# Kernel optimization log

Hardware: AMD Instinct MI355X
Metric: run time of the kernel (lower is better)

## Reference

```python
import jax, jax.numpy as jnp
import numpy as np
import math

B, N, DQ, DK, DV, H = 8, 1024, 512, 512, 512, 8


def setup_inputs() -> dict:
    key = jax.random.key(0)
    ks = jax.random.split(key, 9)
    s = 0.02
    return {
        "Q": jax.random.normal(ks[0], (B, N, DQ), jnp.float32),
        "K": jax.random.normal(ks[1], (B, N, DK), jnp.float32),
        "mask": jax.random.bernoulli(ks[2], 0.9, (B, N)).astype(jnp.float32),
        "Wq": jax.random.normal(ks[3], (DQ, DV), jnp.float32) * s,
        "bq": jnp.zeros((DV,), jnp.float32),
        "Wk": jax.random.normal(ks[4], (DK, DV), jnp.float32) * s,
        "bk": jnp.zeros((DV,), jnp.float32),
        "Wv": jax.random.normal(ks[5], (DK, DV), jnp.float32) * s,
        "bv": jnp.zeros((DV,), jnp.float32),
        "Wo": jax.random.normal(ks[6], (DV, DV), jnp.float32) * s,
        "bo": jnp.zeros((DV,), jnp.float32),
    }


def reference(Q, K, mask, Wq, bq, Wk, bk, Wv, bv, Wo, bo):
    b, n, _ = Q.shape
    dV = Wq.shape[1]
    dh = dV // H
    scale = 1.0 / math.sqrt(dV)
    m = mask[..., None]                      # [B,N,1]
    Qp = (Q @ Wq + bq) * m                   # [B,N,dV]
    Kp = (K @ Wk + bk) * m
    Vp = (K @ Wv + bv) * m
    # torch.cat(x.split(dh,2),0) == head-major stacking -> keep as [H,B,N,dh]
    q = Qp.reshape(b, n, H, dh).transpose(2, 0, 1, 3)
    k = Kp.reshape(b, n, H, dh).transpose(2, 0, 1, 3)
    v = Vp.reshape(b, n, H, dh).transpose(2, 0, 1, 3)
    S = jnp.einsum('hbnd,hbmd->hbnm', q, k) * scale   # [H,B,N,N]
    mx = jnp.max(S, axis=3, keepdims=True)            # unmasked row max (faithful)
    m1 = mask[None, :, :, None]                       # [1,B,N,1]
    m2 = mask[None, :, None, :]                       # [1,B,1,N]
    num = jnp.exp((S - mx) * m1 * m2) * m1 * m2
    A = num / (jnp.sum(num, axis=3, keepdims=True) + 1e-16)
    O = q + jnp.einsum('hbnm,hbmd->hbnd', A, v)       # residual on Q_
    O = O.transpose(1, 2, 0, 3).reshape(b, n, dV)     # un-split heads
    O = O + jax.nn.relu((O @ Wo + bo) * m)
    return O
```

## Files before the change

kernel.cpp:

```cpp
#include <hip/hip_runtime.h>

typedef short bf16x8 __attribute__((ext_vector_type(8)));
typedef float f32x4 __attribute__((ext_vector_type(4)));

#define MFMA16(a, b, c) __builtin_amdgcn_mfma_f32_16x16x32_bf16((a), (b), (c), 0, 0, 0)

#define GLOAD_LDS16(g, l)                                              \
  __builtin_amdgcn_global_load_lds(                                    \
      (const __attribute__((address_space(1))) unsigned int*)(g),      \
      (__attribute__((address_space(3))) unsigned int*)(l), 16, 0, 0)

__device__ __forceinline__ unsigned short f2b(float f) {
  union { float f; unsigned int u; } x; x.f = f;
  unsigned int r = x.u + 0x7FFFu + ((x.u >> 16) & 1u);
  return (unsigned short)(r >> 16);
}
__device__ __forceinline__ float b2f(unsigned short h) {
  union { unsigned int u; float f; } x; x.u = ((unsigned int)h) << 16;
  return x.f;
}
__device__ __forceinline__ unsigned int cvtpk(float lo, float hi) {
  unsigned int r;
  asm("v_cvt_pk_bf16_f32 %0, %1, %2" : "=v"(r) : "v"(lo), "v"(hi));
  return r;
}
__device__ __forceinline__ short cvt1(float x) {
  return (short)(unsigned short)cvtpk(x, x);
}
__device__ __forceinline__ float vexp2(float x) {
  float r;
  asm("v_exp_f32 %0, %1" : "=v"(r) : "v"(x));
  return r;
}

__global__ __launch_bounds__(256) void wtrans_kernel(
    const float* __restrict__ Wq, const float* __restrict__ Wk,
    const float* __restrict__ Wv, const float* __restrict__ Wo,
    short* __restrict__ Wt) {
  __shared__ float tile[64][65];
  const int z = blockIdx.z;
  const float* W = (z == 0) ? Wq : (z == 1) ? Wk : (z == 2) ? Wv : Wo;
  const int k0 = blockIdx.x * 64, n0 = blockIdx.y * 64;
  const int t = threadIdx.x;
  const int r = t >> 4, cc = (t & 15) * 4;
#pragma unroll
  for (int it = 0; it < 4; ++it) {
    int row = r + it * 16;
    const float4 v = *(const float4*)(W + (k0 + row) * 512 + n0 + cc);
    tile[row][cc + 0] = v.x; tile[row][cc + 1] = v.y;
    tile[row][cc + 2] = v.z; tile[row][cc + 3] = v.w;
  }
  __syncthreads();
  short* out = Wt + z * (512 * 512);
#pragma unroll
  for (int it = 0; it < 4; ++it) {
    int nrow = r + it * 16;
    unsigned int u0 = cvtpk(tile[cc + 0][nrow], tile[cc + 1][nrow]);
    unsigned int u1 = cvtpk(tile[cc + 2][nrow], tile[cc + 3][nrow]);
    uint2 uv; uv.x = u0; uv.y = u1;
    *(uint2*)(out + (n0 + nrow) * 512 + k0 + cc) = uv;
  }
}

__global__ __launch_bounds__(256) void cvt_kernel(
    const float* __restrict__ Q, const float* __restrict__ K,
    const float* __restrict__ mask,
    short* __restrict__ Qb, short* __restrict__ Kb, float* __restrict__ ml) {
  if (blockIdx.y == 0 && blockIdx.x < 4) {
    int i = (blockIdx.x * 256 + threadIdx.x) * 8;
    float4 a = *(const float4*)(mask + i);
    float4 bb = *(const float4*)(mask + i + 4);
    float4 ra, rb;
    ra.x = (a.x != 0.f) ? 0.f : -1e30f;
    ra.y = (a.y != 0.f) ? 0.f : -1e30f;
    ra.z = (a.z != 0.f) ? 0.f : -1e30f;
    ra.w = (a.w != 0.f) ? 0.f : -1e30f;
    rb.x = (bb.x != 0.f) ? 0.f : -1e30f;
    rb.y = (bb.y != 0.f) ? 0.f : -1e30f;
    rb.z = (bb.z != 0.f) ? 0.f : -1e30f;
    rb.w = (bb.w != 0.f) ? 0.f : -1e30f;
    *(float4*)(ml + i) = ra;
    *(float4*)(ml + i + 4) = rb;
  }
  const float* src = blockIdx.y ? K : Q;
  short* dst = blockIdx.y ? Kb : Qb;
  int i = (blockIdx.x * 256 + threadIdx.x) * 8;
  float4 v0 = *(const float4*)(src + i);
  float4 v1 = *(const float4*)(src + i + 4);
  uint2 a, b;
  a.x = cvtpk(v0.x, v0.y); a.y = cvtpk(v0.z, v0.w);
  b.x = cvtpk(v1.x, v1.y); b.y = cvtpk(v1.z, v1.w);
  *(uint2*)(dst + i) = a;
  *(uint2*)(dst + i + 4) = b;
}

__device__ __forceinline__ void gemm_bf16_core(
    const short* __restrict__ A, const short* __restrict__ Wt,
    short* Lb, int m0, int t, f32x4 acc[4][4]) {
  const int lane = t & 63, w = t >> 6;
  const int c = lane & 15, g = lane >> 4;
  const int wr = w >> 1, wc = w & 1;
  const int lr = lane >> 3;
  const int sswz = ((lane & 7) ^ lr) << 3;
  const int swc = (c & 7) << 3;
  short* Al = Lb;
  short* Bl = Lb + 8192;

  for (int kt = 0; kt < 8; ++kt) {
#pragma unroll
    for (int it = 0; it < 4; ++it) {
      int row = w * 32 + it * 8;
      GLOAD_LDS16(A + (size_t)(m0 + row + lr) * 512 + kt * 64 + sswz, Al + row * 64);
      GLOAD_LDS16(Wt + (size_t)(row + lr) * 512 + kt * 64 + sswz, Bl + row * 64);
    }
    __syncthreads();
    __builtin_amdgcn_s_setprio(1);
#pragma unroll
    for (int kc = 0; kc < 2; ++kc) {
      bf16x8 af[4], bfr[4];
#pragma unroll
      for (int mi = 0; mi < 4; ++mi) {
        int r = wr * 64 + mi * 16 + c;
        af[mi] = *(const bf16x8*)(Al + r * 64 + ((kc * 32 + 8 * g) ^ swc));
      }
#pragma unroll
      for (int ni = 0; ni < 4; ++ni) {
        int r = wc * 64 + ni * 16 + c;
        bfr[ni] = *(const bf16x8*)(Bl + r * 64 + ((kc * 32 + 8 * g) ^ swc));
      }
#pragma unroll
      for (int mi = 0; mi < 4; ++mi)
#pragma unroll
        for (int ni = 0; ni < 4; ++ni)
          acc[mi][ni] = MFMA16(af[mi], bfr[ni], acc[mi][ni]);
    }
    __builtin_amdgcn_s_setprio(0);
    __syncthreads();
  }
}

__global__ __launch_bounds__(256) void proj2_kernel(
    const short* __restrict__ Qb, const short* __restrict__ Kb,
    const short* __restrict__ Wt4,
    const float* __restrict__ bq, const float* __restrict__ bk, const float* __restrict__ bv,
    const float* __restrict__ maskf,
    short* __restrict__ Qp, short* __restrict__ Kp, short* __restrict__ Vt) {
  __shared__ short Lbuf[16384];
  const int by = blockIdx.y;
  const int m0 = blockIdx.x * 128;
  const int t = threadIdx.x;
  const short* A;
  const short* Wt;
  const float* bias;
  int nbase;
  if (by < 4) { A = Qb; nbase = by * 128; Wt = Wt4 + nbase * 512; bias = bq; }
  else if (by < 8) { A = Kb; nbase = (by - 4) * 128; Wt = Wt4 + 262144 + nbase * 512; bias = bk; }
  else { A = Kb; nbase = (by - 8) * 128; Wt = Wt4 + 524288 + nbase * 512; bias = bv; }

  const f32x4 zz = {0.f, 0.f, 0.f, 0.f};
  f32x4 acc[4][4];
#pragma unroll
  for (int mi = 0; mi < 4; ++mi)
#pragma unroll
    for (int ni = 0; ni < 4; ++ni) acc[mi][ni] = zz;
  gemm_bf16_core(A, Wt, Lbuf, m0, t, acc);

  const int lane = t & 63, w = t >> 6;
  const int c = lane & 15, g = lane >> 4;
  const int wr = w >> 1, wc = w & 1;
  float mk[4][4];
#pragma unroll
  for (int mi = 0; mi < 4; ++mi) {
    int mbase = m0 + wr * 64 + mi * 16 + 4 * g;
#pragma unroll
    for (int i = 0; i < 4; ++i) mk[mi][i] = maskf[mbase + i];
  }
  float bval[4];
#pragma unroll
  for (int ni = 0; ni < 4; ++ni) bval[ni] = bias[nbase + wc * 64 + ni * 16 + c];

  if (by < 8) {
#pragma unroll
    for (int ni = 0; ni < 4; ++ni) {
      int nloc = wc * 64 + ni * 16 + c;
#pragma unroll
      for (int mi = 0; mi < 4; ++mi) {
#pragma unroll
        for (int i = 0; i < 4; ++i) {
          int mloc = wr * 64 + mi * 16 + 4 * g + i;
          float v = (acc[mi][ni][i] + bval[ni]) * mk[mi][i];
          Lbuf[mloc * 128 + (nloc ^ ((mloc & 7) << 3))] = cvt1(v);
        }
      }
    }
    __syncthreads();
    short* outp = (by < 4) ? Qp : Kp;
    const int rrow = t >> 4, rcol = (t & 15) * 8;
#pragma unroll
    for (int p = 0; p < 8; ++p) {
      int m = p * 16 + rrow;
      bf16x8 vv = *(const bf16x8*)(Lbuf + m * 128 + (rcol ^ ((m & 7) << 3)));
      *(bf16x8*)(outp + (size_t)(m0 + m) * 512 + nbase + rcol) = vv;
    }
  } else {
#pragma unroll
    for (int ni = 0; ni < 4; ++ni) {
      int nloc = wc * 64 + ni * 16 + c;
#pragma unroll
      for (int mi = 0; mi < 4; ++mi) {
        int mloc4 = wr * 64 + mi * 16 + 4 * g;
        unsigned int lo = cvtpk((acc[mi][ni][0] + bval[ni]) * mk[mi][0],
                                (acc[mi][ni][1] + bval[ni]) * mk[mi][1]);
        unsigned int hi = cvtpk((acc[mi][ni][2] + bval[ni]) * mk[mi][2],
                                (acc[mi][ni][3] + bval[ni]) * mk[mi][3]);
        int ma = (mloc4 & 15) + (((mloc4 >> 4) ^ (nloc & 7)) << 4);
        uint2 uv; uv.x = lo; uv.y = hi;
        *(uint2*)(Lbuf + nloc * 128 + ma) = uv;
      }
    }
    __syncthreads();
    const int rrow = t >> 4, rcol = (t & 15) * 8;
#pragma unroll
    for (int p = 0; p < 8; ++p) {
      int n = p * 16 + rrow;
      int ma = (rcol & 8) + (((rcol >> 4) ^ (n & 7)) << 4);
      bf16x8 vv = *(const bf16x8*)(Lbuf + n * 128 + ma);
      int d = nbase + n;
      int hh = d >> 6, dd = d & 63;
      int mg = m0 + rcol;
      int bi = mg >> 10, seq0 = mg & 1023;
      *(bf16x8*)(Vt + ((size_t)((bi * 8 + hh) * 64 + dd)) * 1024 + seq0) = vv;
    }
  }
}

__global__ __launch_bounds__(128) void attn3_kernel(
    const short* __restrict__ Qp, const short* __restrict__ Kp,
    const short* __restrict__ Vt, const float* __restrict__ mask,
    const float* __restrict__ ml, short* __restrict__ Obb) {
  __shared__ short Kl[64][64];
  __shared__ short Vl[64][64];
  __shared__ short Pl[2][2][16][64];
  __shared__ float Mlds[1024];
  const int t = threadIdx.x, lane = t & 63, w = t >> 6;
  const int c = lane & 15, g = lane >> 4;
  const int hw = blockIdx.x;
  const int L = (hw & 7) * 128 + (hw >> 3);
  const int qt = L & 15, hb = L >> 4;
  const int b = hb & 7, h = hb >> 3;
  const int n0 = qt * 64;
  const float scale2 = 0.06375870724f;

  const short* Kg = Kp + (size_t)(b * 1024) * 512 + h * 64;
  const short* Vg = Vt + (size_t)((b * 8 + h) * 64) * 1024;
  const float* Lg = ml + b * 1024;
  const int sswz = ((lane & 7) ^ (lane >> 3)) << 3;
  const int swc = (c & 7) << 3;

  bf16x8 qf[2][2];
#pragma unroll
  for (int grp = 0; grp < 2; ++grp) {
    const short* qptr = Qp + ((size_t)(b * 1024 + n0 + w * 32 + grp * 16 + c) * 512 + h * 64 + 8 * g);
    qf[grp][0] = *(const bf16x8*)qptr;
    qf[grp][1] = *(const bf16x8*)(qptr + 32);
  }
  bf16x8 ones;
#pragma unroll
  for (int k = 0; k < 8; ++k) ones[k] = (short)0x3F80;

  auto STAGEKV = [&](int kvt) {
    const int kr = kvt * 64;
#pragma unroll
    for (int it = 0; it < 4; ++it) {
      int row = it * 16 + w * 8;
      GLOAD_LDS16(Kg + (size_t)(kr + row + (lane >> 3)) * 512 + sswz, &Kl[row][0]);
      GLOAD_LDS16(Vg + (size_t)(row + (lane >> 3)) * 1024 + kr + sswz, &Vl[row][0]);
    }
  };

  GLOAD_LDS16(Lg + w * 512 + lane * 4, &Mlds[w * 512]);
  GLOAD_LDS16(Lg + w * 512 + 256 + lane * 4, &Mlds[w * 512 + 256]);
  STAGEKV(0);
  __syncthreads();

  const f32x4 zz = {0.f, 0.f, 0.f, 0.f};
  f32x4 o[2][4];
  f32x4 suma[2];
#pragma unroll
  for (int grp = 0; grp < 2; ++grp) {
    suma[grp] = zz;
#pragma unroll
    for (int nb = 0; nb < 4; ++nb) o[grp][nb] = zz;
  }

#pragma unroll 1
  for (int kvt = 0; kvt < 16; ++kvt) {
    float4 lm[4];
#pragma unroll
    for (int j = 0; j < 4; ++j)
      lm[j] = *(const float4*)(&Mlds[kvt * 64 + 16 * j + 4 * g]);

    f32x4 sv[2][4];
    __builtin_amdgcn_s_setprio(1);
#pragma unroll
    for (int j = 0; j < 4; ++j) {
      bf16x8 af0 = *(const bf16x8*)(&Kl[16 * j + c][(8 * g) ^ swc]);
      bf16x8 af1 = *(const bf16x8*)(&Kl[16 * j + c][(32 + 8 * g) ^ swc]);
#pragma unroll
      for (int grp = 0; grp < 2; ++grp) {
        f32x4 sj = MFMA16(af0, qf[grp][0], zz);
        sv[grp][j] = MFMA16(af1, qf[grp][1], sj);
      }
    }
    __builtin_amdgcn_s_setprio(0);

#pragma unroll
    for (int grp = 0; grp < 2; ++grp) {
#pragma unroll
      for (int j = 0; j < 4; ++j) {
        float p0 = vexp2(fmaf(scale2, sv[grp][j][0], lm[j].x));
        float p1 = vexp2(fmaf(scale2, sv[grp][j][1], lm[j].y));
        float p2 = vexp2(fmaf(scale2, sv[grp][j][2], lm[j].z));
        float p3 = vexp2(fmaf(scale2, sv[grp][j][3], lm[j].w));
        uint2 pw; pw.x = cvtpk(p0, p1); pw.y = cvtpk(p2, p3);
        *(uint2*)(&Pl[w][grp][c][(16 * j + 4 * g) ^ swc]) = pw;
      }
    }

    __builtin_amdgcn_s_setprio(1);
#pragma unroll
    for (int ks = 0; ks < 2; ++ks) {
      bf16x8 vb[4];
#pragma unroll
      for (int nb = 0; nb < 4; ++nb)
        vb[nb] = *(const bf16x8*)(&Vl[16 * nb + c][(ks * 32 + 8 * g) ^ swc]);
#pragma unroll
      for (int grp = 0; grp < 2; ++grp) {
        bf16x8 pa = *(const bf16x8*)(&Pl[w][grp][c][(ks * 32 + 8 * g) ^ swc]);
        suma[grp] = MFMA16(pa, ones, suma[grp]);
#pragma unroll
        for (int nb = 0; nb < 4; ++nb)
          o[grp][nb] = MFMA16(pa, vb[nb], o[grp][nb]);
      }
    }
    __builtin_amdgcn_s_setprio(0);

    if (kvt < 15) {
      __syncthreads();
      STAGEKV(kvt + 1);
      __syncthreads();
    }
  }

#pragma unroll
  for (int grp = 0; grp < 2; ++grp) {
    float inv[4], mk1[4];
#pragma unroll
    for (int i = 0; i < 4; ++i) {
      inv[i] = __builtin_amdgcn_rcpf(suma[grp][i] + 1e-16f);
      mk1[i] = mask[b * 1024 + n0 + w * 32 + grp * 16 + 4 * g + i];
    }
#pragma unroll
    for (int nb = 0; nb < 4; ++nb) {
      int colg = h * 64 + 16 * nb + c;
#pragma unroll
      for (int i = 0; i < 4; ++i) {
        int row = n0 + w * 32 + grp * 16 + 4 * g + i;
        float att = o[grp][nb][i] * inv[i];
        float qv = b2f(*(const unsigned short*)(Qp + (size_t)(b * 1024 + row) * 512 + colg));
        float res = qv + mk1[i] * att;
        Obb[(size_t)(b * 1024 + row) * 512 + colg] = cvt1(res);
      }
    }
  }
}

__global__ __launch_bounds__(256) void final2_kernel(
    const short* __restrict__ Obb,
    const short* __restrict__ Wto, const float* __restrict__ bo,
    const float* __restrict__ maskf, float* __restrict__ out) {
  __shared__ short Lbuf[16384];
  const int m0 = blockIdx.x * 128, n0 = blockIdx.y * 128;
  const int t = threadIdx.x;
  const f32x4 zz = {0.f, 0.f, 0.f, 0.f};
  f32x4 acc[4][4];
#pragma unroll
  for (int mi = 0; mi < 4; ++mi)
#pragma unroll
    for (int ni = 0; ni < 4; ++ni) acc[mi][ni] = zz;
  gemm_bf16_core(Obb, Wto + n0 * 512, Lbuf, m0, t, acc);

  const int lane = t & 63, w = t >> 6;
  const int c = lane & 15, g = lane >> 4;
  const int wr = w >> 1, wc = w & 1;
  float mk[4][4];
#pragma unroll
  for (int mi = 0; mi < 4; ++mi) {
    int mbase = m0 + wr * 64 + mi * 16 + 4 * g;
#pragma unroll
    for (int i = 0; i < 4; ++i) mk[mi][i] = maskf[mbase + i];
  }
#pragma unroll
  for (int ni = 0; ni < 4; ++ni) {
    int n = n0 + wc * 64 + ni * 16 + c;
    float bval = bo[n];
#pragma unroll
    for (int mi = 0; mi < 4; ++mi) {
      int mbase = m0 + wr * 64 + mi * 16 + 4 * g;
#pragma unroll
      for (int i = 0; i < 4; ++i) {
        float v = (acc[mi][ni][i] + bval) * mk[mi][i];
        v = fmaxf(v, 0.f);
        size_t off = (size_t)(mbase + i) * 512 + n;
        out[off] = b2f((unsigned short)Obb[off]) + v;
      }
    }
  }
}

extern "C" void kernel_launch(void* const* d_in, const int* in_sizes, int n_in,
                              void* d_out, int out_size, void* d_ws, size_t ws_size,
                              hipStream_t stream) {
  (void)in_sizes; (void)n_in; (void)out_size; (void)ws_size;
  const float* Q    = (const float*)d_in[0];
  const float* K    = (const float*)d_in[1];
  const float* mask = (const float*)d_in[2];
  const float* Wq   = (const float*)d_in[3];
  const float* bq   = (const float*)d_in[4];
  const float* Wk   = (const float*)d_in[5];
  const float* bk   = (const float*)d_in[6];
  const float* Wv   = (const float*)d_in[7];
  const float* bv   = (const float*)d_in[8];
  const float* Wo   = (const float*)d_in[9];
  const float* bo   = (const float*)d_in[10];

  char* ws = (char*)d_ws;
  const size_t MB = 1048576;
  short* Wt4 = (short*)ws;
  short* Qb  = (short*)(ws + 2 * MB);
  short* Kb  = (short*)(ws + 10 * MB);
  short* Qp  = (short*)(ws + 18 * MB);
  short* Kp  = (short*)(ws + 26 * MB);
  short* Vt  = (short*)(ws + 34 * MB);
  short* Obb = (short*)(ws + 42 * MB);
  float* ml  = (float*)(ws + 50 * MB);
  float* out = (float*)d_out;

  wtrans_kernel<<<dim3(8, 8, 4), 256, 0, stream>>>(Wq, Wk, Wv, Wo, Wt4);
  cvt_kernel<<<dim3(2048, 2), 256, 0, stream>>>(Q, K, mask, Qb, Kb, ml);
  proj2_kernel<<<dim3(64, 12), 256, 0, stream>>>(Qb, Kb, Wt4, bq, bk, bv, mask, Qp, Kp, Vt);
  attn3_kernel<<<dim3(1024), 128, 0, stream>>>(Qp, Kp, Vt, mask, ml, Obb);
  final2_kernel<<<dim3(64, 4), 256, 0, stream>>>(Obb, Wt4 + 3 * 262144, bo, mask, out);
}
```

Baseline: 88.90 us.

## Rewrite attention with 32x32 MFMA single-wave tiles and register-resident probabilities

Replaces the two-wave 16x16 MFMA attention kernel with a one-wave-per-block kernel using 32x32x16 bf16 MFMA on 32-query tiles. The softmax scale is folded into the Wk weights and bias, so scores feed exp2 directly. The additive -1e30 mask is replaced by a bf16 0/1 mask vector used in an MFMA row-sum. This works because masked keys already project to zero K and V, so they add nothing to P·V. Probabilities are repacked across lanes with shuffles instead of going through LDS. The next K/V tile is prefetched right after the LDS reads, with no block barriers. The aim is to cut LDS traffic, syncs and MFMA issue count. The costs are halved blocks per tile, more waves to launch, and a transpose through LDS in the epilogue.

```diff
diff --git a/kernel.cpp b/kernel.cpp
--- a/kernel.cpp
+++ b/kernel.cpp
@@ -2,8 +2,10 @@
 
 typedef short bf16x8 __attribute__((ext_vector_type(8)));
 typedef float f32x4 __attribute__((ext_vector_type(4)));
+typedef float f32x16 __attribute__((ext_vector_type(16)));
 
 #define MFMA16(a, b, c) __builtin_amdgcn_mfma_f32_16x16x32_bf16((a), (b), (c), 0, 0, 0)
+#define MFMA32(a, b, c) __builtin_amdgcn_mfma_f32_32x32x16_bf16((a), (b), (c), 0, 0, 0)
 
 #define GLOAD_LDS16(g, l)                                              \
   __builtin_amdgcn_global_load_lds(                                    \
@@ -32,6 +34,8 @@
   asm("v_exp_f32 %0, %1" : "=v"(r) : "v"(x));
   return r;
 }
+
+#define SCALE2 0.06375870724f
 
 __global__ __launch_bounds__(256) void wtrans_kernel(
     const float* __restrict__ Wq, const float* __restrict__ Wk,
@@ -40,6 +44,7 @@
   __shared__ float tile[64][65];
   const int z = blockIdx.z;
   const float* W = (z == 0) ? Wq : (z == 1) ? Wk : (z == 2) ? Wv : Wo;
+  const float ws = (z == 1) ? SCALE2 : 1.0f;
   const int k0 = blockIdx.x * 64, n0 = blockIdx.y * 64;
   const int t = threadIdx.x;
   const int r = t >> 4, cc = (t & 15) * 4;
@@ -55,8 +60,8 @@
 #pragma unroll
   for (int it = 0; it < 4; ++it) {
     int nrow = r + it * 16;
-    unsigned int u0 = cvtpk(tile[cc + 0][nrow], tile[cc + 1][nrow]);
-    unsigned int u1 = cvtpk(tile[cc + 2][nrow], tile[cc + 3][nrow]);
+    unsigned int u0 = cvtpk(tile[cc + 0][nrow] * ws, tile[cc + 1][nrow] * ws);
+    unsigned int u1 = cvtpk(tile[cc + 2][nrow] * ws, tile[cc + 3][nrow] * ws);
     uint2 uv; uv.x = u0; uv.y = u1;
     *(uint2*)(out + (n0 + nrow) * 512 + k0 + cc) = uv;
   }
@@ -65,22 +70,23 @@
 __global__ __launch_bounds__(256) void cvt_kernel(
     const float* __restrict__ Q, const float* __restrict__ K,
     const float* __restrict__ mask,
-    short* __restrict__ Qb, short* __restrict__ Kb, float* __restrict__ ml) {
+    short* __restrict__ Qb, short* __restrict__ Kb, short* __restrict__ mbf) {
   if (blockIdx.y == 0 && blockIdx.x < 4) {
     int i = (blockIdx.x * 256 + threadIdx.x) * 8;
     float4 a = *(const float4*)(mask + i);
     float4 bb = *(const float4*)(mask + i + 4);
-    float4 ra, rb;
-    ra.x = (a.x != 0.f) ? 0.f : -1e30f;
-    ra.y = (a.y != 0.f) ? 0.f : -1e30f;
-    ra.z = (a.z != 0.f) ? 0.f : -1e30f;
-    ra.w = (a.w != 0.f) ? 0.f : -1e30f;
-    rb.x = (bb.x != 0.f) ? 0.f : -1e30f;
-    rb.y = (bb.y != 0.f) ? 0.f : -1e30f;
-    rb.z = (bb.z != 0.f) ? 0.f : -1e30f;
-    rb.w = (bb.w != 0.f) ? 0.f : -1e30f;
-    *(float4*)(ml + i) = ra;
-    *(float4*)(ml + i + 4) = rb;
+    unsigned int m0 = (a.x != 0.f) ? 0x3F80u : 0u;
+    unsigned int m1 = (a.y != 0.f) ? 0x3F80u : 0u;
+    unsigned int m2 = (a.z != 0.f) ? 0x3F80u : 0u;
+    unsigned int m3 = (a.w != 0.f) ? 0x3F80u : 0u;
+    unsigned int m4 = (bb.x != 0.f) ? 0x3F80u : 0u;
+    unsigned int m5 = (bb.y != 0.f) ? 0x3F80u : 0u;
+    unsigned int m6 = (bb.z != 0.f) ? 0x3F80u : 0u;
+    unsigned int m7 = (bb.w != 0.f) ? 0x3F80u : 0u;
+    uint4 mm;
+    mm.x = m0 | (m1 << 16); mm.y = m2 | (m3 << 16);
+    mm.z = m4 | (m5 << 16); mm.w = m6 | (m7 << 16);
+    *(uint4*)(mbf + i) = mm;
   }
   const float* src = blockIdx.y ? K : Q;
   short* dst = blockIdx.y ? Kb : Qb;
@@ -156,6 +162,7 @@
   if (by < 4) { A = Qb; nbase = by * 128; Wt = Wt4 + nbase * 512; bias = bq; }
   else if (by < 8) { A = Kb; nbase = (by - 4) * 128; Wt = Wt4 + 262144 + nbase * 512; bias = bk; }
   else { A = Kb; nbase = (by - 8) * 128; Wt = Wt4 + 524288 + nbase * 512; bias = bv; }
+  const float bscale = (by >= 4 && by < 8) ? SCALE2 : 1.0f;
 
   const f32x4 zz = {0.f, 0.f, 0.f, 0.f};
   f32x4 acc[4][4];
@@ -177,7 +184,7 @@
   }
   float bval[4];
 #pragma unroll
-  for (int ni = 0; ni < 4; ++ni) bval[ni] = bias[nbase + wc * 64 + ni * 16 + c];
+  for (int ni = 0; ni < 4; ++ni) bval[ni] = bias[nbase + wc * 64 + ni * 16 + c] * bscale;
 
   if (by < 8) {
 #pragma unroll
@@ -234,144 +241,165 @@
   }
 }
 
-__global__ __launch_bounds__(128) void attn3_kernel(
+__global__ __launch_bounds__(64) void attn4_kernel(
     const short* __restrict__ Qp, const short* __restrict__ Kp,
     const short* __restrict__ Vt, const float* __restrict__ mask,
-    const float* __restrict__ ml, short* __restrict__ Obb) {
+    const short* __restrict__ mbf, short* __restrict__ Obb) {
   __shared__ short Kl[64][64];
   __shared__ short Vl[64][64];
-  __shared__ short Pl[2][2][16][64];
-  __shared__ float Mlds[1024];
-  const int t = threadIdx.x, lane = t & 63, w = t >> 6;
-  const int c = lane & 15, g = lane >> 4;
+  __shared__ short Ml[1024];
+  __shared__ short Tl[32][68];
+  const int t = threadIdx.x;
+  const int q32 = t & 31, hi = t >> 5;
   const int hw = blockIdx.x;
-  const int L = (hw & 7) * 128 + (hw >> 3);
-  const int qt = L & 15, hb = L >> 4;
-  const int b = hb & 7, h = hb >> 3;
-  const int n0 = qt * 64;
-  const float scale2 = 0.06375870724f;
+  const int L = (hw & 7) * 256 + (hw >> 3);
+  const int qt = L & 31, head = L >> 5;
+  const int b = head & 7, h = head >> 3;
+  const int n0 = qt * 32;
 
   const short* Kg = Kp + (size_t)(b * 1024) * 512 + h * 64;
   const short* Vg = Vt + (size_t)((b * 8 + h) * 64) * 1024;
-  const float* Lg = ml + b * 1024;
-  const int sswz = ((lane & 7) ^ (lane >> 3)) << 3;
-  const int swc = (c & 7) << 3;
-
-  bf16x8 qf[2][2];
-#pragma unroll
-  for (int grp = 0; grp < 2; ++grp) {
-    const short* qptr = Qp + ((size_t)(b * 1024 + n0 + w * 32 + grp * 16 + c) * 512 + h * 64 + 8 * g);
-    qf[grp][0] = *(const bf16x8*)qptr;
-    qf[grp][1] = *(const bf16x8*)(qptr + 32);
-  }
-  bf16x8 ones;
-#pragma unroll
-  for (int k = 0; k < 8; ++k) ones[k] = (short)0x3F80;
-
-  auto STAGEKV = [&](int kvt) {
+  const int sswz = ((t & 7) ^ (t >> 3)) << 3;
+  const int rswz = (t & 7) << 3;
+
+  bf16x8 qf[4];
+  {
+    const short* qptr = Qp + ((size_t)(b * 1024 + n0 + q32) * 512 + h * 64 + 8 * hi);
+#pragma unroll
+    for (int kk = 0; kk < 4; ++kk) qf[kk] = *(const bf16x8*)(qptr + 16 * kk);
+  }
+
+  auto STAGE = [&](int kvt) {
     const int kr = kvt * 64;
 #pragma unroll
-    for (int it = 0; it < 4; ++it) {
-      int row = it * 16 + w * 8;
-      GLOAD_LDS16(Kg + (size_t)(kr + row + (lane >> 3)) * 512 + sswz, &Kl[row][0]);
-      GLOAD_LDS16(Vg + (size_t)(row + (lane >> 3)) * 1024 + kr + sswz, &Vl[row][0]);
+    for (int it = 0; it < 8; ++it) {
+      int row = it * 8;
+      GLOAD_LDS16(Kg + (size_t)(kr + row + (t >> 3)) * 512 + sswz, &Kl[row][0]);
+      GLOAD_LDS16(Vg + (size_t)(row + (t >> 3)) * 1024 + kr + sswz, &Vl[row][0]);
     }
   };
 
-  GLOAD_LDS16(Lg + w * 512 + lane * 4, &Mlds[w * 512]);
-  GLOAD_LDS16(Lg + w * 512 + 256 + lane * 4, &Mlds[w * 512 + 256]);
-  STAGEKV(0);
-  __syncthreads();
-
-  const f32x4 zz = {0.f, 0.f, 0.f, 0.f};
-  f32x4 o[2][4];
-  f32x4 suma[2];
-#pragma unroll
-  for (int grp = 0; grp < 2; ++grp) {
-    suma[grp] = zz;
-#pragma unroll
-    for (int nb = 0; nb < 4; ++nb) o[grp][nb] = zz;
-  }
+  GLOAD_LDS16(mbf + b * 1024 + t * 8, &Ml[0]);
+  GLOAD_LDS16(mbf + b * 1024 + 512 + t * 8, &Ml[512]);
+  STAGE(0);
+
+  f32x16 o0 = {0.f}, o1 = {0.f}, suma = {0.f};
+#pragma unroll
+  for (int e = 0; e < 16; ++e) { o0[e] = 0.f; o1[e] = 0.f; suma[e] = 0.f; }
 
 #pragma unroll 1
   for (int kvt = 0; kvt < 16; ++kvt) {
-    float4 lm[4];
-#pragma unroll
-    for (int j = 0; j < 4; ++j)
-      lm[j] = *(const float4*)(&Mlds[kvt * 64 + 16 * j + 4 * g]);
-
-    f32x4 sv[2][4];
+    asm volatile("s_waitcnt vmcnt(0)" ::: "memory");
+    __builtin_amdgcn_sched_barrier(0);
+
+    bf16x8 ka[2][4], va[2][4], mo[4];
+#pragma unroll
+    for (int nb = 0; nb < 2; ++nb)
+#pragma unroll
+      for (int kk = 0; kk < 4; ++kk)
+        ka[nb][kk] = *(const bf16x8*)(&Kl[32 * nb + q32][(16 * kk + 8 * hi) ^ rswz]);
+#pragma unroll
+    for (int ds = 0; ds < 2; ++ds)
+#pragma unroll
+      for (int kk = 0; kk < 4; ++kk)
+        va[ds][kk] = *(const bf16x8*)(&Vl[32 * ds + q32][(16 * kk + 8 * hi) ^ rswz]);
+#pragma unroll
+    for (int kk = 0; kk < 4; ++kk)
+      mo[kk] = *(const bf16x8*)(&Ml[kvt * 64 + 16 * kk + 8 * hi]);
+
+    __builtin_amdgcn_sched_barrier(0);
+    asm volatile("s_waitcnt lgkmcnt(0)" ::: "memory");
+    __builtin_amdgcn_sched_barrier(0);
+    if (kvt < 15) STAGE(kvt + 1);
+    __builtin_amdgcn_sched_barrier(0);
+
+    f32x16 s0 = {0.f}, s1 = {0.f};
+#pragma unroll
+    for (int e = 0; e < 16; ++e) { s0[e] = 0.f; s1[e] = 0.f; }
     __builtin_amdgcn_s_setprio(1);
 #pragma unroll
-    for (int j = 0; j < 4; ++j) {
-      bf16x8 af0 = *(const bf16x8*)(&Kl[16 * j + c][(8 * g) ^ swc]);
-      bf16x8 af1 = *(const bf16x8*)(&Kl[16 * j + c][(32 + 8 * g) ^ swc]);
-#pragma unroll
-      for (int grp = 0; grp < 2; ++grp) {
-        f32x4 sj = MFMA16(af0, qf[grp][0], zz);
-        sv[grp][j] = MFMA16(af1, qf[grp][1], sj);
-      }
-    }
+    for (int kk = 0; kk < 4; ++kk) s0 = MFMA32(ka[0][kk], qf[kk], s0);
+#pragma unroll
+    for (int kk = 0; kk < 4; ++kk) s1 = MFMA32(ka[1][kk], qf[kk], s1);
     __builtin_amdgcn_s_setprio(0);
 
-#pragma unroll
-    for (int grp = 0; grp < 2; ++grp) {
-#pragma unroll
-      for (int j = 0; j < 4; ++j) {
-        float p0 = vexp2(fmaf(scale2, sv[grp][j][0], lm[j].x));
-        float p1 = vexp2(fmaf(scale2, sv[grp][j][1], lm[j].y));
-        float p2 = vexp2(fmaf(scale2, sv[grp][j][2], lm[j].z));
-        float p3 = vexp2(fmaf(scale2, sv[grp][j][3], lm[j].w));
-        uint2 pw; pw.x = cvtpk(p0, p1); pw.y = cvtpk(p2, p3);
-        *(uint2*)(&Pl[w][grp][c][(16 * j + 4 * g) ^ swc]) = pw;
-      }
+    f32x16 p0, p1;
+#pragma unroll
+    for (int e = 0; e < 16; ++e) p0[e] = vexp2(s0[e]);
+#pragma unroll
+    for (int e = 0; e < 16; ++e) p1[e] = vexp2(s1[e]);
+
+    bf16x8 pf[4];
+#pragma unroll
+    for (int kk = 0; kk < 4; ++kk) {
+      const int m_ = kk & 1;
+      unsigned int w01a, w01b, w23a, w23b;
+      if (kk < 2) {
+        w01a = cvtpk(p0[8 * m_ + 0], p0[8 * m_ + 1]);
+        w01b = cvtpk(p0[8 * m_ + 2], p0[8 * m_ + 3]);
+        w23a = cvtpk(p0[8 * m_ + 4], p0[8 * m_ + 5]);
+        w23b = cvtpk(p0[8 * m_ + 6], p0[8 * m_ + 7]);
+      } else {
+        w01a = cvtpk(p1[8 * m_ + 0], p1[8 * m_ + 1]);
+        w01b = cvtpk(p1[8 * m_ + 2], p1[8 * m_ + 3]);
+        w23a = cvtpk(p1[8 * m_ + 4], p1[8 * m_ + 5]);
+        w23b = cvtpk(p1[8 * m_ + 6], p1[8 * m_ + 7]);
+      }
+      unsigned int x0 = hi ? w01a : w23a;
+      unsigned int x1 = hi ? w01b : w23b;
+      unsigned int g0 = (unsigned int)__shfl_xor((int)x0, 32);
+      unsigned int g1 = (unsigned int)__shfl_xor((int)x1, 32);
+      union { unsigned int u[4]; bf16x8 v; } pu;
+      pu.u[0] = hi ? g0 : w01a;
+      pu.u[1] = hi ? g1 : w01b;
+      pu.u[2] = hi ? w23a : g0;
+      pu.u[3] = hi ? w23b : g1;
+      pf[kk] = pu.v;
     }
 
     __builtin_amdgcn_s_setprio(1);
 #pragma unroll
-    for (int ks = 0; ks < 2; ++ks) {
-      bf16x8 vb[4];
-#pragma unroll
-      for (int nb = 0; nb < 4; ++nb)
-        vb[nb] = *(const bf16x8*)(&Vl[16 * nb + c][(ks * 32 + 8 * g) ^ swc]);
-#pragma unroll
-      for (int grp = 0; grp < 2; ++grp) {
-        bf16x8 pa = *(const bf16x8*)(&Pl[w][grp][c][(ks * 32 + 8 * g) ^ swc]);
-        suma[grp] = MFMA16(pa, ones, suma[grp]);
-#pragma unroll
-        for (int nb = 0; nb < 4; ++nb)
-          o[grp][nb] = MFMA16(pa, vb[nb], o[grp][nb]);
-      }
-    }
+    for (int kk = 0; kk < 4; ++kk) o0 = MFMA32(va[0][kk], pf[kk], o0);
+#pragma unroll
+    for (int kk = 0; kk < 4; ++kk) o1 = MFMA32(va[1][kk], pf[kk], o1);
+#pragma unroll
+    for (int kk = 0; kk < 4; ++kk) suma = MFMA32(mo[kk], pf[kk], suma);
     __builtin_amdgcn_s_setprio(0);
-
-    if (kvt < 15) {
-      __syncthreads();
-      STAGEKV(kvt + 1);
-      __syncthreads();
-    }
-  }
-
-#pragma unroll
-  for (int grp = 0; grp < 2; ++grp) {
-    float inv[4], mk1[4];
-#pragma unroll
-    for (int i = 0; i < 4; ++i) {
-      inv[i] = __builtin_amdgcn_rcpf(suma[grp][i] + 1e-16f);
-      mk1[i] = mask[b * 1024 + n0 + w * 32 + grp * 16 + 4 * g + i];
-    }
-#pragma unroll
-    for (int nb = 0; nb < 4; ++nb) {
-      int colg = h * 64 + 16 * nb + c;
-#pragma unroll
-      for (int i = 0; i < 4; ++i) {
-        int row = n0 + w * 32 + grp * 16 + 4 * g + i;
-        float att = o[grp][nb][i] * inv[i];
-        float qv = b2f(*(const unsigned short*)(Qp + (size_t)(b * 1024 + row) * 512 + colg));
-        float res = qv + mk1[i] * att;
-        Obb[(size_t)(b * 1024 + row) * 512 + colg] = cvt1(res);
-      }
-    }
+  }
+
+  const float inv = __builtin_amdgcn_rcpf(suma[0] + 1e-16f);
+#pragma unroll
+  for (int rr = 0; rr < 4; ++rr) {
+    unsigned int lo0 = cvtpk(o0[4 * rr + 0] * inv, o0[4 * rr + 1] * inv);
+    unsigned int hi0 = cvtpk(o0[4 * rr + 2] * inv, o0[4 * rr + 3] * inv);
+    uint2 uv0; uv0.x = lo0; uv0.y = hi0;
+    *(uint2*)(&Tl[q32][8 * rr + 4 * hi]) = uv0;
+    unsigned int lo1 = cvtpk(o1[4 * rr + 0] * inv, o1[4 * rr + 1] * inv);
+    unsigned int hi1 = cvtpk(o1[4 * rr + 2] * inv, o1[4 * rr + 3] * inv);
+    uint2 uv1; uv1.x = lo1; uv1.y = hi1;
+    *(uint2*)(&Tl[q32][32 + 8 * rr + 4 * hi]) = uv1;
+  }
+  asm volatile("s_waitcnt lgkmcnt(0)" ::: "memory");
+  __builtin_amdgcn_sched_barrier(0);
+
+  const int erow = t >> 1, ecs = (t & 1) * 8;
+  const float mk1 = mask[b * 1024 + n0 + erow];
+#pragma unroll
+  for (int it = 0; it < 4; ++it) {
+    int col = ecs + it * 16;
+    bf16x8 av = *(const bf16x8*)(&Tl[erow][col]);
+    const short* qptr = Qp + (size_t)(b * 1024 + n0 + erow) * 512 + h * 64 + col;
+    bf16x8 qv = *(const bf16x8*)qptr;
+    uint4 rr;
+    rr.x = cvtpk(b2f((unsigned short)qv[0]) + mk1 * b2f((unsigned short)av[0]),
+                 b2f((unsigned short)qv[1]) + mk1 * b2f((unsigned short)av[1]));
+    rr.y = cvtpk(b2f((unsigned short)qv[2]) + mk1 * b2f((unsigned short)av[2]),
+                 b2f((unsigned short)qv[3]) + mk1 * b2f((unsigned short)av[3]));
+    rr.z = cvtpk(b2f((unsigned short)qv[4]) + mk1 * b2f((unsigned short)av[4]),
+                 b2f((unsigned short)qv[5]) + mk1 * b2f((unsigned short)av[5]));
+    rr.w = cvtpk(b2f((unsigned short)qv[6]) + mk1 * b2f((unsigned short)av[6]),
+                 b2f((unsigned short)qv[7]) + mk1 * b2f((unsigned short)av[7]));
+    *(uint4*)(Obb + (size_t)(b * 1024 + n0 + erow) * 512 + h * 64 + col) = rr;
   }
 }
 
@@ -443,12 +471,12 @@
   short* Kp  = (short*)(ws + 26 * MB);
   short* Vt  = (short*)(ws + 34 * MB);
   short* Obb = (short*)(ws + 42 * MB);
-  float* ml  = (float*)(ws + 50 * MB);
+  short* mbf = (short*)(ws + 50 * MB);
   float* out = (float*)d_out;
 
   wtrans_kernel<<<dim3(8, 8, 4), 256, 0, stream>>>(Wq, Wk, Wv, Wo, Wt4);
-  cvt_kernel<<<dim3(2048, 2), 256, 0, stream>>>(Q, K, mask, Qb, Kb, ml);
+  cvt_kernel<<<dim3(2048, 2), 256, 0, stream>>>(Q, K, mask, Qb, Kb, mbf);
   proj2_kernel<<<dim3(64, 12), 256, 0, stream>>>(Qb, Kb, Wt4, bq, bk, bv, mask, Qp, Kp, Vt);
-  attn3_kernel<<<dim3(1024), 128, 0, stream>>>(Qp, Kp, Vt, mask, ml, Obb);
+  attn4_kernel<<<dim3(2048), 64, 0, stream>>>(Qp, Kp, Vt, mask, mbf, Obb);
   final2_kernel<<<dim3(64, 4), 256, 0, stream>>>(Obb, Wt4 + 3 * 262144, bo, mask, out);
 }
```

Measured after the change: 103.4 us. 16.3% more time.
